# Performance work log

Hardware: AMD Instinct MI355X
Metric: run time of the kernel (lower is better)

Reference implementation:

```python
import jax, jax.numpy as jnp
import numpy as np

EPS = 1e-5  # torch BatchNorm2d default eps


def setup_inputs() -> dict:
    key = jax.random.key(0)
    ks = jax.random.split(key, 11)
    n, c, h, w = 16, 512, 64, 64
    grp, cg, mip = 4, 128, 16
    return {
        "x": jax.random.normal(ks[0], (n, c, h, w), dtype=jnp.float32),
        "W1": jax.random.normal(ks[1], (mip, cg), dtype=jnp.float32) * 0.05,
        "b1": jax.random.normal(ks[2], (mip,), dtype=jnp.float32) * 0.05,
        "gamma": jax.random.uniform(ks[3], (mip,), dtype=jnp.float32, minval=0.5, maxval=1.5),
        "beta": jax.random.normal(ks[4], (mip,), dtype=jnp.float32) * 0.05,
        "mean": jax.random.normal(ks[5], (mip,), dtype=jnp.float32) * 0.05,
        "var": jax.random.uniform(ks[6], (mip,), dtype=jnp.float32, minval=0.5, maxval=1.5),
        "Wh": jax.random.normal(ks[7], (cg, mip), dtype=jnp.float32) * 0.1,
        "bh": jax.random.normal(ks[8], (cg,), dtype=jnp.float32) * 0.05,
        "Ww": jax.random.normal(ks[9], (cg, mip), dtype=jnp.float32) * 0.1,
        "bw": jax.random.normal(ks[10], (cg,), dtype=jnp.float32) * 0.05,
    }


def reference(x, W1, b1, gamma, beta, mean, var, Wh, bh, Ww, bw):
    n, c, h, w = x.shape
    grp = 4
    cg = c // grp
    # Since c % 4 == 0, torch.split gives 4 equal groups: fold group into a new axis.
    xg = x.reshape(n, grp, cg, h, w)                       # (n,g,cg,h,w)
    gh = xg.mean(axis=4)                                   # pool over w -> (n,g,cg,h)
    gw = xg.mean(axis=3)                                   # pool over h -> (n,g,cg,w)
    y = jnp.concatenate([gh, gw], axis=3)                  # (n,g,cg,h+w)
    # conv1 (1x1) shared across all 4 groups
    y = jnp.einsum('ngcl,mc->ngml', y, W1) + b1[None, None, :, None]
    # BatchNorm2d (eval mode, running stats)
    scale = gamma / jnp.sqrt(var + EPS)
    y = y * scale[None, None, :, None] + (beta - mean * scale)[None, None, :, None]
    # h_swish: x * relu6(x+3)/6
    y = y * (jnp.clip(y + 3.0, 0.0, 6.0) / 6.0)
    yh, yw = y[..., :h], y[..., h:]                        # (n,g,mip,h), (n,g,mip,w)
    a_h = jax.nn.sigmoid(jnp.einsum('ngml,cm->ngcl', yh, Wh) + bh[None, None, :, None])
    a_w = jax.nn.sigmoid(jnp.einsum('ngml,cm->ngcl', yw, Ww) + bw[None, None, :, None])
    out = xg * a_h[..., :, None] * a_w[..., None, :]       # (n,g,cg,h,w)
    out = out.reshape(n, c, h, w)
    # channel shuffle: (n, cg, grp, h, w) -> permute group axis forward
    out = out.reshape(n, cg, grp, h, w).transpose(0, 2, 1, 3, 4).reshape(n, c, h, w)
    return out
```

## Files before the change

kernel.cpp:

```cpp
#include <hip/hip_runtime.h>

#define N_   16
#define C_   512
#define H_   64
#define W_   64
#define GRP  4
#define CG   128
#define MIP  16

__device__ __forceinline__ float bf_lo(unsigned u) { return __uint_as_float(u << 16); }
__device__ __forceinline__ float bf_hi(unsigned u) { return __uint_as_float(u & 0xFFFF0000u); }
__device__ __forceinline__ float bf1(unsigned short s) { return __uint_as_float((unsigned)s << 16); }

__device__ __forceinline__ float ld_scalar(const void* p, int i, bool isbf) {
    return isbf ? bf1(((const unsigned short*)p)[i]) : ((const float*)p)[i];
}

__device__ __forceinline__ bool sniff_isbf(const unsigned* __restrict__ x32,
                                           int t, unsigned* s_flag) {
    if (t < 64) {
        int cnt = 0;
        #pragma unroll
        for (int k = 0; k < 4; ++k) {
            unsigned w = x32[t + 64 * k];
            unsigned e = (w >> 7) & 0xFFu;
            cnt += (e >= 0x60u && e <= 0x9Fu) ? 1 : 0;
        }
        #pragma unroll
        for (int off = 32; off > 0; off >>= 1) cnt += __shfl_down(cnt, off, 64);
        if (t == 0) *s_flag = (cnt >= 192) ? 1u : 0u;
    }
    __syncthreads();
    return *s_flag != 0u;
}

__global__ __launch_bounds__(256) void kreduce(const void* __restrict__ xv,
                                               float* __restrict__ gh,
                                               float* __restrict__ gw) {
    __shared__ float tile[64 * 65];
    __shared__ unsigned flag_s;
    const int bid = blockIdx.x;
    const int t = threadIdx.x;
    const bool isbf = sniff_isbf((const unsigned*)xv, t, &flag_s);

    if (isbf) {
        const uint4* src = (const uint4*)((const unsigned short*)xv + (size_t)bid * 4096);
        #pragma unroll
        for (int half = 0; half < 2; ++half) {
            int idx = t + half * 256;
            int r = idx >> 3;
            int j0 = (idx & 7) * 8;
            uint4 v = src[idx];
            unsigned uu[4] = {v.x, v.y, v.z, v.w};
            #pragma unroll
            for (int k = 0; k < 4; ++k) {
                tile[r * 65 + j0 + 2 * k]     = bf_lo(uu[k]);
                tile[r * 65 + j0 + 2 * k + 1] = bf_hi(uu[k]);
            }
        }
    } else {
        const float4* src = (const float4*)((const float*)xv + (size_t)bid * 4096);
        #pragma unroll
        for (int it = 0; it < 4; ++it) {
            int idx = t + it * 256;
            int r = idx >> 4;
            int j0 = (idx & 15) * 4;
            float4 v = src[idx];
            tile[r * 65 + j0]     = v.x;
            tile[r * 65 + j0 + 1] = v.y;
            tile[r * 65 + j0 + 2] = v.z;
            tile[r * 65 + j0 + 3] = v.w;
        }
    }
    __syncthreads();

    if (t < 64) {
        float s = 0.f;
        #pragma unroll
        for (int j = 0; j < 64; ++j) s += tile[t * 65 + j];
        gh[(size_t)bid * 64 + t] = s * (1.0f / 64.0f);
    } else if (t < 128) {
        int j = t - 64;
        float s = 0.f;
        #pragma unroll
        for (int i = 0; i < 64; ++i) s += tile[i * 65 + j];
        gw[(size_t)bid * 64 + j] = s * (1.0f / 64.0f);
    }
}

__global__ __launch_bounds__(256) void ky(
    const void* __restrict__ xv,
    const float* __restrict__ gh, const float* __restrict__ gw,
    const void* __restrict__ W1, const void* __restrict__ b1,
    const void* __restrict__ gamma, const void* __restrict__ beta,
    const void* __restrict__ mean, const void* __restrict__ var,
    float* __restrict__ y)
{
    __shared__ float W1_s[MIP * CG];
    __shared__ float scale_s[MIP], shift_s[MIP], b1_s[MIP];
    __shared__ unsigned flag_s;

    const int t = threadIdx.x;
    const bool isbf = sniff_isbf((const unsigned*)xv, t, &flag_s);

    if (isbf) {
        uint4 v = ((const uint4*)W1)[t];
        unsigned uu[4] = {v.x, v.y, v.z, v.w};
        #pragma unroll
        for (int k = 0; k < 4; ++k) {
            W1_s[t * 8 + 2 * k]     = bf_lo(uu[k]);
            W1_s[t * 8 + 2 * k + 1] = bf_hi(uu[k]);
        }
    } else {
        #pragma unroll
        for (int it = 0; it < 2; ++it) {
            int idx = t + 256 * it;
            float4 v = ((const float4*)W1)[idx];
            W1_s[idx * 4]     = v.x;
            W1_s[idx * 4 + 1] = v.y;
            W1_s[idx * 4 + 2] = v.z;
            W1_s[idx * 4 + 3] = v.w;
        }
    }
    if (t < MIP) {
        float sc = ld_scalar(gamma, t, isbf) * rsqrtf(ld_scalar(var, t, isbf) + 1e-5f);
        scale_s[t] = sc;
        shift_s[t] = ld_scalar(beta, t, isbf) - ld_scalar(mean, t, isbf) * sc;
        b1_s[t] = ld_scalar(b1, t, isbf);
    }
    __syncthreads();

    const int l = t & 127;
    const int half = t >> 7;
    const size_t base = (size_t)blockIdx.x * (CG * 64);
    const float* src = (l < 64) ? (gh + base + l) : (gw + base + (l - 64));
    float acc[8] = {0.f, 0.f, 0.f, 0.f, 0.f, 0.f, 0.f, 0.f};
    for (int cc = 0; cc < CG; ++cc) {
        float v = src[(size_t)cc * 64];
        #pragma unroll
        for (int mm = 0; mm < 8; ++mm)
            acc[mm] += W1_s[(half * 8 + mm) * CG + cc] * v;
    }
    float* yb = y + (size_t)blockIdx.x * (MIP * 128);
    #pragma unroll
    for (int mm = 0; mm < 8; ++mm) {
        int m = half * 8 + mm;
        float yv = acc[mm] + b1_s[m];
        yv = yv * scale_s[m] + shift_s[m];
        float hc = fminf(fmaxf(yv + 3.0f, 0.0f), 6.0f);
        yb[m * 128 + l] = yv * hc * (1.0f / 6.0f);
    }
}

__global__ __launch_bounds__(256) void kapply(const void* __restrict__ xv,
                                              const float* __restrict__ y,
                                              const void* __restrict__ Wh,
                                              const void* __restrict__ bh,
                                              const void* __restrict__ Ww,
                                              const void* __restrict__ bw,
                                              void* __restrict__ outv) {
    __shared__ float ah_s[64], aw_s[64];
    __shared__ unsigned flag_s;
    const int bid = blockIdx.x;
    const int n = bid >> 9;
    const int o = bid & 511;
    const int g2 = o >> 7, cc2 = o & 127;
    const int p = cc2 * 4 + g2;
    const int g = p >> 7, cc = p & 127;
    const int t = threadIdx.x;
    const bool isbf = sniff_isbf((const unsigned*)xv, t, &flag_s);

    if (t < 128) {
        const int i = t & 63;
        const bool isW = (t >= 64);
        const void* Wp = isW ? Ww : Wh;
        const void* bp = isW ? bw : bh;
        const float* ysrc = y + (size_t)(n * 4 + g) * (MIP * 128) + (isW ? 64 : 0) + i;
        float acc = ld_scalar(bp, cc, isbf);
        #pragma unroll
        for (int m = 0; m < MIP; ++m)
            acc += ld_scalar(Wp, cc * MIP + m, isbf) * ysrc[m * 128];
        float s = 1.0f / (1.0f + __expf(-acc));
        if (isW) aw_s[i] = s; else ah_s[i] = s;
    }
    __syncthreads();

    if (isbf) {
        const uint4* src = (const uint4*)((const unsigned short*)xv + ((size_t)n * 512 + p) * 4096);
        uint4* dst = (uint4*)((unsigned short*)outv + (size_t)bid * 4096);
        #pragma unroll
        for (int half = 0; half < 2; ++half) {
            int idx = t + half * 256;
            int r = idx >> 3;
            int j0 = (idx & 7) * 8;
            float sah = ah_s[r];
            uint4 v = src[idx];
            unsigned uu[4] = {v.x, v.y, v.z, v.w};
            unsigned res[4];
            #pragma unroll
            for (int k = 0; k < 4; ++k) {
                int j = j0 + 2 * k;
                float f0 = bf_lo(uu[k]) * sah * aw_s[j];
                float f1 = bf_hi(uu[k]) * sah * aw_s[j + 1];
                unsigned u0 = __float_as_uint(f0); u0 += 0x7FFFu + ((u0 >> 16) & 1u);
                unsigned u1 = __float_as_uint(f1); u1 += 0x7FFFu + ((u1 >> 16) & 1u);
                res[k] = (u0 >> 16) | (u1 & 0xFFFF0000u);
            }
            uint4 w; w.x = res[0]; w.y = res[1]; w.z = res[2]; w.w = res[3];
            dst[idx] = w;
        }
    } else {
        const float4* src = (const float4*)((const float*)xv + ((size_t)n * 512 + p) * 4096);
        float4* dst = (float4*)((float*)outv + (size_t)bid * 4096);
        #pragma unroll
        for (int it = 0; it < 4; ++it) {
            int idx = t + it * 256;
            int r = idx >> 4;
            int j0 = (idx & 15) * 4;
            float sah = ah_s[r];
            float4 v = src[idx];
            v.x *= sah * aw_s[j0];
            v.y *= sah * aw_s[j0 + 1];
            v.z *= sah * aw_s[j0 + 2];
            v.w *= sah * aw_s[j0 + 3];
            dst[idx] = v;
        }
    }
}

extern "C" void kernel_launch(void* const* d_in, const int* in_sizes, int n_in,
                              void* d_out, int out_size, void* d_ws, size_t ws_size,
                              hipStream_t stream) {
    const void* x     = d_in[0];
    const void* W1    = d_in[1];
    const void* b1    = d_in[2];
    const void* gamma = d_in[3];
    const void* beta  = d_in[4];
    const void* mean  = d_in[5];
    const void* var   = d_in[6];
    const void* Wh    = d_in[7];
    const void* bh    = d_in[8];
    const void* Ww    = d_in[9];
    const void* bw    = d_in[10];

    float* ws = (float*)d_ws;
    const size_t seg = (size_t)N_ * GRP * CG * 64;
    float* gh = ws;
    float* gw = gh + seg;
    float* yv = gw + seg;

    kreduce<<<N_ * C_, 256, 0, stream>>>(x, gh, gw);
    ky<<<N_ * GRP, 256, 0, stream>>>(x, gh, gw, W1, b1, gamma, beta, mean, var, yv);
    kapply<<<N_ * C_, 256, 0, stream>>>(x, yv, Wh, bh, Ww, bw, d_out);
}
```

Measured before the change: 277.8 us.

## Fuse three kernels into one cooperative persistent kernel with grid syncs

Replaces the three launches (reduce, conv1/BN/hswish, apply) with a single cooperative kernel that loops over tiles persistently and separates the phases with grid.sync. Grid size comes from the occupancy query and is capped at 1024 blocks. The aim is to remove launch overhead and inter-kernel gaps. The tradeoffs are that phase 2 runs on only 64 blocks while the rest of the grid waits, and that the fixed grid cap and grid-wide barriers may lower achieved bandwidth in the memory-bound phases.

```diff
diff --git a/kernel.cpp b/kernel.cpp
--- a/kernel.cpp
+++ b/kernel.cpp
@@ -1,12 +1,15 @@
 #include <hip/hip_runtime.h>
+#include <hip/hip_cooperative_groups.h>
+
+namespace cg = cooperative_groups;
 
 #define N_   16
 #define C_   512
-#define H_   64
-#define W_   64
 #define GRP  4
 #define CG   128
 #define MIP  16
+#define TPB  256
+#define NTILE (N_ * C_)
 
 __device__ __forceinline__ float bf_lo(unsigned u) { return __uint_as_float(u << 16); }
 __device__ __forceinline__ float bf_hi(unsigned u) { return __uint_as_float(u & 0xFFFF0000u); }
@@ -34,58 +37,223 @@
     return *s_flag != 0u;
 }
 
-__global__ __launch_bounds__(256) void kreduce(const void* __restrict__ xv,
-                                               float* __restrict__ gh,
-                                               float* __restrict__ gw) {
-    __shared__ float tile[64 * 65];
-    __shared__ unsigned flag_s;
-    const int bid = blockIdx.x;
-    const int t = threadIdx.x;
-    const bool isbf = sniff_isbf((const unsigned*)xv, t, &flag_s);
-
+
+__device__ __forceinline__ void phase1_tile(const void* xv, bool isbf, int bid,
+                                            int t, float* smem,
+                                            float* gh, float* gw) {
     if (isbf) {
         const uint4* src = (const uint4*)((const unsigned short*)xv + (size_t)bid * 4096);
         #pragma unroll
-        for (int half = 0; half < 2; ++half) {
-            int idx = t + half * 256;
+        for (int hh = 0; hh < 2; ++hh) {
+            int idx = t + hh * 256;
             int r = idx >> 3;
             int j0 = (idx & 7) * 8;
             uint4 v = src[idx];
             unsigned uu[4] = {v.x, v.y, v.z, v.w};
             #pragma unroll
             for (int k = 0; k < 4; ++k) {
-                tile[r * 65 + j0 + 2 * k]     = bf_lo(uu[k]);
-                tile[r * 65 + j0 + 2 * k + 1] = bf_hi(uu[k]);
+                smem[r * 65 + j0 + 2 * k]     = bf_lo(uu[k]);
+                smem[r * 65 + j0 + 2 * k + 1] = bf_hi(uu[k]);
             }
         }
     } else {
         const float4* src = (const float4*)((const float*)xv + (size_t)bid * 4096);
         #pragma unroll
-        for (int it = 0; it < 4; ++it) {
-            int idx = t + it * 256;
+        for (int q = 0; q < 4; ++q) {
+            int idx = t + q * 256;
             int r = idx >> 4;
             int j0 = (idx & 15) * 4;
             float4 v = src[idx];
-            tile[r * 65 + j0]     = v.x;
-            tile[r * 65 + j0 + 1] = v.y;
-            tile[r * 65 + j0 + 2] = v.z;
-            tile[r * 65 + j0 + 3] = v.w;
-        }
-    }
-    __syncthreads();
-
+            smem[r * 65 + j0]     = v.x;
+            smem[r * 65 + j0 + 1] = v.y;
+            smem[r * 65 + j0 + 2] = v.z;
+            smem[r * 65 + j0 + 3] = v.w;
+        }
+    }
+    __syncthreads();
     if (t < 64) {
         float s = 0.f;
         #pragma unroll
-        for (int j = 0; j < 64; ++j) s += tile[t * 65 + j];
+        for (int j = 0; j < 64; ++j) s += smem[t * 65 + j];
         gh[(size_t)bid * 64 + t] = s * (1.0f / 64.0f);
     } else if (t < 128) {
         int j = t - 64;
         float s = 0.f;
         #pragma unroll
-        for (int i = 0; i < 64; ++i) s += tile[i * 65 + j];
+        for (int i = 0; i < 64; ++i) s += smem[i * 65 + j];
         gw[(size_t)bid * 64 + j] = s * (1.0f / 64.0f);
     }
+    __syncthreads();
+}
+
+__device__ __forceinline__ void phase2_y(bool isbf, int ng, int t, float* smem,
+                                         const float* gh, const float* gw,
+                                         const void* W1, const void* b1,
+                                         const void* gamma, const void* beta,
+                                         const void* mean, const void* var,
+                                         float* y) {
+    float* W1_s    = smem;
+    float* scale_s = smem + 2048;
+    float* shift_s = smem + 2064;
+    float* b1_s    = smem + 2080;
+
+    if (isbf) {
+        uint4 v = ((const uint4*)W1)[t];
+        unsigned uu[4] = {v.x, v.y, v.z, v.w};
+        #pragma unroll
+        for (int k = 0; k < 4; ++k) {
+            W1_s[t * 8 + 2 * k]     = bf_lo(uu[k]);
+            W1_s[t * 8 + 2 * k + 1] = bf_hi(uu[k]);
+        }
+    } else {
+        #pragma unroll
+        for (int q = 0; q < 2; ++q) {
+            int idx = t + 256 * q;
+            float4 v = ((const float4*)W1)[idx];
+            W1_s[idx * 4]     = v.x;
+            W1_s[idx * 4 + 1] = v.y;
+            W1_s[idx * 4 + 2] = v.z;
+            W1_s[idx * 4 + 3] = v.w;
+        }
+    }
+    if (t < MIP) {
+        float sc = ld_scalar(gamma, t, isbf) * rsqrtf(ld_scalar(var, t, isbf) + 1e-5f);
+        scale_s[t] = sc;
+        shift_s[t] = ld_scalar(beta, t, isbf) - ld_scalar(mean, t, isbf) * sc;
+        b1_s[t] = ld_scalar(b1, t, isbf);
+    }
+    __syncthreads();
+
+    const int l = t & 127;
+    const int half = t >> 7;
+    const size_t base = (size_t)ng * (CG * 64);
+    const float* src = (l < 64) ? (gh + base + l) : (gw + base + (l - 64));
+    float acc[8] = {0.f, 0.f, 0.f, 0.f, 0.f, 0.f, 0.f, 0.f};
+    for (int cc = 0; cc < CG; ++cc) {
+        float v = src[(size_t)cc * 64];
+        #pragma unroll
+        for (int mm = 0; mm < 8; ++mm)
+            acc[mm] += W1_s[(half * 8 + mm) * CG + cc] * v;
+    }
+    float* yb = y + (size_t)ng * (MIP * 128);
+    #pragma unroll
+    for (int mm = 0; mm < 8; ++mm) {
+        int m = half * 8 + mm;
+        float yv = acc[mm] + b1_s[m];
+        yv = yv * scale_s[m] + shift_s[m];
+        float hc = fminf(fmaxf(yv + 3.0f, 0.0f), 6.0f);
+        yb[m * 128 + l] = yv * hc * (1.0f / 6.0f);
+    }
+    __syncthreads();
+}
+
+__device__ __forceinline__ void phase3_tile(const void* xv, bool isbf, int bid,
+                                            int t, float* smem, const float* y,
+                                            const void* Wh, const void* bh,
+                                            const void* Ww, const void* bw,
+                                            void* outv) {
+    const int n = bid >> 9;
+    const int o = bid & 511;
+    const int g2 = o >> 7, cc2 = o & 127;
+    const int p = cc2 * 4 + g2;
+    const int g = p >> 7, cc = p & 127;
+
+    if (t < 128) {
+        const int i = t & 63;
+        const bool isW = (t >= 64);
+        const void* Wp = isW ? Ww : Wh;
+        const void* bp = isW ? bw : bh;
+        const float* ysrc = y + (size_t)(n * 4 + g) * (MIP * 128) + (isW ? 64 : 0) + i;
+        float acc = ld_scalar(bp, cc, isbf);
+        #pragma unroll
+        for (int m = 0; m < MIP; ++m)
+            acc += ld_scalar(Wp, cc * MIP + m, isbf) * ysrc[m * 128];
+        smem[t] = 1.0f / (1.0f + __expf(-acc));
+    }
+    __syncthreads();
+
+    if (isbf) {
+        const uint4* src = (const uint4*)((const unsigned short*)xv + ((size_t)n * 512 + p) * 4096);
+        uint4* dst = (uint4*)((unsigned short*)outv + (size_t)bid * 4096);
+        #pragma unroll
+        for (int hh = 0; hh < 2; ++hh) {
+            int idx = t + hh * 256;
+            int r = idx >> 3;
+            int j0 = (idx & 7) * 8;
+            float sah = smem[r];
+            uint4 v = src[idx];
+            unsigned uu[4] = {v.x, v.y, v.z, v.w};
+            unsigned res[4];
+            #pragma unroll
+            for (int k = 0; k < 4; ++k) {
+                int j = j0 + 2 * k;
+                float f0 = bf_lo(uu[k]) * sah * smem[64 + j];
+                float f1 = bf_hi(uu[k]) * sah * smem[64 + j + 1];
+                unsigned u0 = __float_as_uint(f0); u0 += 0x7FFFu + ((u0 >> 16) & 1u);
+                unsigned u1 = __float_as_uint(f1); u1 += 0x7FFFu + ((u1 >> 16) & 1u);
+                res[k] = (u0 >> 16) | (u1 & 0xFFFF0000u);
+            }
+            uint4 w; w.x = res[0]; w.y = res[1]; w.z = res[2]; w.w = res[3];
+            dst[idx] = w;
+        }
+    } else {
+        const float4* src = (const float4*)((const float*)xv + ((size_t)n * 512 + p) * 4096);
+        float4* dst = (float4*)((float*)outv + (size_t)bid * 4096);
+        #pragma unroll
+        for (int q = 0; q < 4; ++q) {
+            int idx = t + q * 256;
+            int r = idx >> 4;
+            int j0 = (idx & 15) * 4;
+            float sah = smem[r];
+            float4 v = src[idx];
+            v.x *= sah * smem[64 + j0];
+            v.y *= sah * smem[64 + j0 + 1];
+            v.z *= sah * smem[64 + j0 + 2];
+            v.w *= sah * smem[64 + j0 + 3];
+            dst[idx] = v;
+        }
+    }
+    __syncthreads();
+}
+
+__global__ __launch_bounds__(256) void kfused(
+    const void* __restrict__ xv,
+    const void* __restrict__ W1, const void* __restrict__ b1,
+    const void* __restrict__ gamma, const void* __restrict__ beta,
+    const void* __restrict__ mean, const void* __restrict__ var,
+    const void* __restrict__ Wh, const void* __restrict__ bh,
+    const void* __restrict__ Ww, const void* __restrict__ bw,
+    void* __restrict__ outv,
+    float* __restrict__ gh, float* __restrict__ gw, float* __restrict__ y)
+{
+    __shared__ float smem[64 * 65];
+    __shared__ unsigned flag_s;
+    const int t = threadIdx.x;
+    const bool isbf = sniff_isbf((const unsigned*)xv, t, &flag_s);
+    cg::grid_group grid = cg::this_grid();
+
+    for (int bid = blockIdx.x; bid < NTILE; bid += gridDim.x)
+        phase1_tile(xv, isbf, bid, t, smem, gh, gw);
+
+    grid.sync();
+
+    for (int ng = blockIdx.x; ng < N_ * GRP; ng += gridDim.x)
+        phase2_y(isbf, ng, t, smem, gh, gw, W1, b1, gamma, beta, mean, var, y);
+
+    grid.sync();
+
+    for (int bid = blockIdx.x; bid < NTILE; bid += gridDim.x)
+        phase3_tile(xv, isbf, bid, t, smem, y, Wh, bh, Ww, bw, outv);
+}
+
+__global__ __launch_bounds__(256) void kreduce(const void* __restrict__ xv,
+                                               float* __restrict__ gh,
+                                               float* __restrict__ gw) {
+    __shared__ float smem[64 * 65];
+    __shared__ unsigned flag_s;
+    const int t = threadIdx.x;
+    const bool isbf = sniff_isbf((const unsigned*)xv, t, &flag_s);
+    phase1_tile(xv, isbf, blockIdx.x, t, smem, gh, gw);
 }
 
 __global__ __launch_bounds__(256) void ky(
@@ -96,60 +264,11 @@
     const void* __restrict__ mean, const void* __restrict__ var,
     float* __restrict__ y)
 {
-    __shared__ float W1_s[MIP * CG];
-    __shared__ float scale_s[MIP], shift_s[MIP], b1_s[MIP];
+    __shared__ float smem[2112];
     __shared__ unsigned flag_s;
-
     const int t = threadIdx.x;
     const bool isbf = sniff_isbf((const unsigned*)xv, t, &flag_s);
-
-    if (isbf) {
-        uint4 v = ((const uint4*)W1)[t];
-        unsigned uu[4] = {v.x, v.y, v.z, v.w};
-        #pragma unroll
-        for (int k = 0; k < 4; ++k) {
-            W1_s[t * 8 + 2 * k]     = bf_lo(uu[k]);
-            W1_s[t * 8 + 2 * k + 1] = bf_hi(uu[k]);
-        }
-    } else {
-        #pragma unroll
-        for (int it = 0; it < 2; ++it) {
-            int idx = t + 256 * it;
-            float4 v = ((const float4*)W1)[idx];
-            W1_s[idx * 4]     = v.x;
-            W1_s[idx * 4 + 1] = v.y;
-            W1_s[idx * 4 + 2] = v.z;
-            W1_s[idx * 4 + 3] = v.w;
-        }
-    }
-    if (t < MIP) {
-        float sc = ld_scalar(gamma, t, isbf) * rsqrtf(ld_scalar(var, t, isbf) + 1e-5f);
-        scale_s[t] = sc;
-        shift_s[t] = ld_scalar(beta, t, isbf) - ld_scalar(mean, t, isbf) * sc;
-        b1_s[t] = ld_scalar(b1, t, isbf);
-    }
-    __syncthreads();
-
-    const int l = t & 127;
-    const int half = t >> 7;
-    const size_t base = (size_t)blockIdx.x * (CG * 64);
-    const float* src = (l < 64) ? (gh + base + l) : (gw + base + (l - 64));
-    float acc[8] = {0.f, 0.f, 0.f, 0.f, 0.f, 0.f, 0.f, 0.f};
-    for (int cc = 0; cc < CG; ++cc) {
-        float v = src[(size_t)cc * 64];
-        #pragma unroll
-        for (int mm = 0; mm < 8; ++mm)
-            acc[mm] += W1_s[(half * 8 + mm) * CG + cc] * v;
-    }
-    float* yb = y + (size_t)blockIdx.x * (MIP * 128);
-    #pragma unroll
-    for (int mm = 0; mm < 8; ++mm) {
-        int m = half * 8 + mm;
-        float yv = acc[mm] + b1_s[m];
-        yv = yv * scale_s[m] + shift_s[m];
-        float hc = fminf(fmaxf(yv + 3.0f, 0.0f), 6.0f);
-        yb[m * 128 + l] = yv * hc * (1.0f / 6.0f);
-    }
+    phase2_y(isbf, blockIdx.x, t, smem, gh, gw, W1, b1, gamma, beta, mean, var, y);
 }
 
 __global__ __launch_bounds__(256) void kapply(const void* __restrict__ xv,
@@ -159,73 +278,11 @@
                                               const void* __restrict__ Ww,
                                               const void* __restrict__ bw,
                                               void* __restrict__ outv) {
-    __shared__ float ah_s[64], aw_s[64];
+    __shared__ float smem[128];
     __shared__ unsigned flag_s;
-    const int bid = blockIdx.x;
-    const int n = bid >> 9;
-    const int o = bid & 511;
-    const int g2 = o >> 7, cc2 = o & 127;
-    const int p = cc2 * 4 + g2;
-    const int g = p >> 7, cc = p & 127;
     const int t = threadIdx.x;
     const bool isbf = sniff_isbf((const unsigned*)xv, t, &flag_s);
-
-    if (t < 128) {
-        const int i = t & 63;
-        const bool isW = (t >= 64);
-        const void* Wp = isW ? Ww : Wh;
-        const void* bp = isW ? bw : bh;
-        const float* ysrc = y + (size_t)(n * 4 + g) * (MIP * 128) + (isW ? 64 : 0) + i;
-        float acc = ld_scalar(bp, cc, isbf);
-        #pragma unroll
-        for (int m = 0; m < MIP; ++m)
-            acc += ld_scalar(Wp, cc * MIP + m, isbf) * ysrc[m * 128];
-        float s = 1.0f / (1.0f + __expf(-acc));
-        if (isW) aw_s[i] = s; else ah_s[i] = s;
-    }
-    __syncthreads();
-
-    if (isbf) {
-        const uint4* src = (const uint4*)((const unsigned short*)xv + ((size_t)n * 512 + p) * 4096);
-        uint4* dst = (uint4*)((unsigned short*)outv + (size_t)bid * 4096);
-        #pragma unroll
-        for (int half = 0; half < 2; ++half) {
-            int idx = t + half * 256;
-            int r = idx >> 3;
-            int j0 = (idx & 7) * 8;
-            float sah = ah_s[r];
-            uint4 v = src[idx];
-            unsigned uu[4] = {v.x, v.y, v.z, v.w};
-            unsigned res[4];
-            #pragma unroll
-            for (int k = 0; k < 4; ++k) {
-                int j = j0 + 2 * k;
-                float f0 = bf_lo(uu[k]) * sah * aw_s[j];
-                float f1 = bf_hi(uu[k]) * sah * aw_s[j + 1];
-                unsigned u0 = __float_as_uint(f0); u0 += 0x7FFFu + ((u0 >> 16) & 1u);
-                unsigned u1 = __float_as_uint(f1); u1 += 0x7FFFu + ((u1 >> 16) & 1u);
-                res[k] = (u0 >> 16) | (u1 & 0xFFFF0000u);
-            }
-            uint4 w; w.x = res[0]; w.y = res[1]; w.z = res[2]; w.w = res[3];
-            dst[idx] = w;
-        }
-    } else {
-        const float4* src = (const float4*)((const float*)xv + ((size_t)n * 512 + p) * 4096);
-        float4* dst = (float4*)((float*)outv + (size_t)bid * 4096);
-        #pragma unroll
-        for (int it = 0; it < 4; ++it) {
-            int idx = t + it * 256;
-            int r = idx >> 4;
-            int j0 = (idx & 15) * 4;
-            float sah = ah_s[r];
-            float4 v = src[idx];
-            v.x *= sah * aw_s[j0];
-            v.y *= sah * aw_s[j0 + 1];
-            v.z *= sah * aw_s[j0 + 2];
-            v.w *= sah * aw_s[j0 + 3];
-            dst[idx] = v;
-        }
-    }
+    phase3_tile(xv, isbf, blockIdx.x, t, smem, y, Wh, bh, Ww, bw, outv);
 }
 
 extern "C" void kernel_launch(void* const* d_in, const int* in_sizes, int n_in,
@@ -248,8 +305,34 @@
     float* gh = ws;
     float* gw = gh + seg;
     float* yv = gw + seg;
-
-    kreduce<<<N_ * C_, 256, 0, stream>>>(x, gh, gw);
-    ky<<<N_ * GRP, 256, 0, stream>>>(x, gh, gw, W1, b1, gamma, beta, mean, var, yv);
-    kapply<<<N_ * C_, 256, 0, stream>>>(x, yv, Wh, bh, Ww, bw, d_out);
-}
+    void* outp = d_out;
+
+    bool launched = false;
+    int dev = 0;
+    if (hipGetDevice(&dev) == hipSuccess) {
+        int coop = 0, numCU = 0, blocksPerCU = 0;
+        hipDeviceGetAttribute(&coop, hipDeviceAttributeCooperativeLaunch, dev);
+        hipDeviceGetAttribute(&numCU, hipDeviceAttributeMultiprocessorCount, dev);
+        hipOccupancyMaxActiveBlocksPerMultiprocessor(&blocksPerCU,
+                                                     (const void*)kfused, TPB, 0);
+        long nblk = (long)blocksPerCU * (long)numCU;
+        if (nblk > 1024) nblk = 1024;
+        if (coop && nblk >= 1) {
+            void* args[] = {
+                (void*)&x, (void*)&W1, (void*)&b1, (void*)&gamma, (void*)&beta,
+                (void*)&mean, (void*)&var, (void*)&Wh, (void*)&bh, (void*)&Ww,
+                (void*)&bw, (void*)&outp, (void*)&gh, (void*)&gw, (void*)&yv
+            };
+            hipError_t rc = hipLaunchCooperativeKernel((const void*)kfused,
+                                                       dim3((unsigned)nblk),
+                                                       dim3(TPB), args, 0, stream);
+            launched = (rc == hipSuccess);
+        }
+    }
+    if (!launched) {
+        (void)hipGetLastError();
+        kreduce<<<NTILE, TPB, 0, stream>>>(x, gh, gw);
+        ky<<<N_ * GRP, TPB, 0, stream>>>(x, gh, gw, W1, b1, gamma, beta, mean, var, yv);
+        kapply<<<NTILE, TPB, 0, stream>>>(x, yv, Wh, bh, Ww, bw, d_out);
+    }
+}
```

Result: slower. 418.8 us (+50.7%).
